# Performance work log

Hardware: AMD Instinct MI355X
Metric: run time of the kernel (lower is better)

The kernel has to match this reference:

```python
import jax, jax.numpy as jnp
import numpy as np

D_MODEL = 40
NUM_BUCKETS = 32
MAX_DISTANCE = 128
EPS = 1e-6


def rms_norm(x, w):
    # T5 LayerNorm: no mean subtraction, no bias
    var = jnp.mean(jnp.square(x), axis=-1, keepdims=True)
    return x * jax.lax.rsqrt(var + EPS) * w


def relative_position_bucket(rel, num_buckets=NUM_BUCKETS, max_distance=MAX_DISTANCE):
    # bidirectional (encoder) variant of T5's bucketing
    num_buckets = num_buckets // 2
    buckets = (rel > 0).astype(jnp.int32) * num_buckets
    rel = jnp.abs(rel)
    max_exact = num_buckets // 2
    is_small = rel < max_exact
    rel_f = jnp.maximum(rel, 1).astype(jnp.float32)
    large = max_exact + (
        jnp.log(rel_f / max_exact) / np.log(max_distance / max_exact) * (num_buckets - max_exact)
    ).astype(jnp.int32)
    large = jnp.minimum(large, num_buckets - 1)
    return buckets + jnp.where(is_small, rel, large)


def setup_inputs() -> dict:
    key = jax.random.key(0)
    ks = jax.random.split(key, 16)
    B, S, Din, D = 8, 2048, 128, D_MODEL
    w = lambda k, shape: (jax.random.normal(k, shape, dtype=jnp.float32) * 0.02)
    return {
        "embs": jax.random.normal(ks[0], (B, S, Din), dtype=jnp.float32),
        "Wa": w(ks[1], (Din, D)),
        "ba": jnp.zeros((D,), dtype=jnp.float32),
        "ln1": jnp.ones((D,), dtype=jnp.float32),
        "Wq": w(ks[2], (D, D)),
        "Wk": w(ks[3], (D, D)),
        "Wv": w(ks[4], (D, D)),
        "Wo": w(ks[5], (D, D)),
        "ln2": jnp.ones((D,), dtype=jnp.float32),
        "wi": w(ks[6], (D, D)),
        "wo": w(ks[7], (D, D)),
        "lnf": jnp.ones((D,), dtype=jnp.float32),
        "rel_bias": w(ks[8], (NUM_BUCKETS, 1)),  # [num_buckets, n_heads=1]
    }


def reference(embs, Wa, ba, ln1, Wq, Wk, Wv, Wo, ln2, wi, wo, lnf, rel_bias):
    # adapter
    x = jax.nn.relu(embs @ Wa + ba)  # [B,S,D]
    S = x.shape[1]

    # --- self-attention block (1 head, d_kv = d_model, no QK scaling) ---
    h = rms_norm(x, ln1)
    q = h @ Wq  # [B,S,D]
    k = h @ Wk
    v = h @ Wv

    pos = jnp.arange(S)
    rel = pos[None, :] - pos[:, None]           # memory - query, [S,S]
    buckets = relative_position_bucket(rel)      # [S,S]
    pos_bias = rel_bias[buckets][:, :, 0]        # [S,S], head dim squeezed (1 head)

    scores = jnp.einsum("bqd,bkd->bqk", q, k) + pos_bias[None]  # [B,S,S]
    attn = jax.nn.softmax(scores, axis=-1)
    o = jnp.einsum("bqk,bkd->bqd", attn, v) @ Wo
    x = x + o

    # --- feed-forward block ---
    h2 = rms_norm(x, ln2)
    f = jax.nn.relu(h2 @ wi) @ wo
    x = x + f

    return rms_norm(x, lnf)
```

## Files before the change

### kernel.cpp

```cpp
#include <hip/hip_runtime.h>
#include <hip/hip_bf16.h>
#include <math.h>

#define D 40
#define DIN 128
#define S 2048
#define B 8
#define NROWS (B*S)
#define DP 64
#define XSTR 48
#define PSTR 64
#define KSTR 72

typedef __bf16 bf16x8 __attribute__((ext_vector_type(8)));
typedef float f32x16 __attribute__((ext_vector_type(16)));

static __device__ __forceinline__ unsigned short f2bf(float f) {
    unsigned u = __builtin_bit_cast(unsigned, f);
    u += 0x7fff + ((u >> 16) & 1);
    return (unsigned short)(u >> 16);
}
static __device__ __forceinline__ float bf2f(unsigned short h) {
    return __builtin_bit_cast(float, (unsigned)h << 16);
}
static __device__ __forceinline__ bf16x8 ldfrag(const unsigned short* p) {
    return __builtin_bit_cast(bf16x8, *(const uint4*)p);
}
static __device__ __forceinline__ unsigned cvtpk(float lo, float hi) {
    unsigned r;
    asm("v_cvt_pk_bf16_f32 %0, %1, %2" : "=v"(r) : "v"(lo), "v"(hi));
    return r;
}
static __device__ __forceinline__ void plswap(unsigned &a, unsigned &b) {
    asm("v_permlane32_swap_b32 %0, %1" : "+v"(a), "+v"(b));
}

__global__ __launch_bounds__(256) void k0_prep(
    const float* __restrict__ Wa, const float* __restrict__ ba, const float* __restrict__ ln1,
    const float* __restrict__ Wq, const float* __restrict__ Wk, const float* __restrict__ Wv,
    const float* __restrict__ Wo, const float* __restrict__ ln2,
    const float* __restrict__ wi, const float* __restrict__ wo,
    const float* __restrict__ rel_bias,
    unsigned short* __restrict__ waT, unsigned short* __restrict__ wqT,
    unsigned short* __restrict__ wkT, unsigned short* __restrict__ wvT,
    unsigned short* __restrict__ woT, unsigned short* __restrict__ wiT,
    unsigned short* __restrict__ wo2T, float* __restrict__ btab)
{
    int i = blockIdx.x * 256 + threadIdx.x;
    if (i < 64*144) {
        int col = i / 144, k = i - col*144;
        float v = 0.f;
        if (col < D) {
            if (k < DIN) v = Wa[k*D + col];
            else if (k == DIN) v = ba[col];
        }
        waT[i] = f2bf(v);
    }
    if (i < 64*48) {
        int col = i / 48, d = i - col*48;
        bool ok = (col < D && d < D);
        float s1 = ok ? ln1[d] : 0.f;
        float s2 = ok ? ln2[d] : 0.f;
        wqT[i]  = f2bf(ok ? Wq[d*D + col] * s1 : 0.f);
        wkT[i]  = f2bf(ok ? Wk[d*D + col] * s1 : 0.f);
        wvT[i]  = f2bf(ok ? Wv[d*D + col] * s1 : 0.f);
        woT[i]  = f2bf(ok ? Wo[d*D + col]      : 0.f);
        wiT[i]  = f2bf(ok ? wi[d*D + col] * s2 : 0.f);
        wo2T[i] = f2bf(ok ? wo[d*D + col]      : 0.f);
    }
    if (i < 2*S - 1) {
        int rel = i - (S - 1);
        int bucket = (rel > 0) ? 16 : 0;
        int ar = rel < 0 ? -rel : rel;
        int add;
        if (ar < 8) {
            add = ar;
        } else {
            float tt = logf((float)ar * 0.125f) / logf(16.0f) * 8.0f;
            int lg = 8 + (int)tt;
            add = lg < 15 ? lg : 15;
        }
        btab[i] = rel_bias[bucket + add];
    }
}

static __device__ __forceinline__ void repack1(const f32x16& t0, uint4& u0, uint4& u1)
{
    unsigned a0=cvtpk(t0[0],t0[1]),  a1=cvtpk(t0[2],t0[3]),
             a2=cvtpk(t0[4],t0[5]),  a3=cvtpk(t0[6],t0[7]);
    plswap(a0,a2); plswap(a1,a3);
    unsigned b0=cvtpk(t0[8],t0[9]),  b1=cvtpk(t0[10],t0[11]),
             b2=cvtpk(t0[12],t0[13]),b3=cvtpk(t0[14],t0[15]);
    plswap(b0,b2); plswap(b1,b3);
    u0 = (uint4){a0,a1,a2,a3}; u1 = (uint4){b0,b1,b2,b3};
}

__global__ __launch_bounds__(128) void k1_adapter_qkv(
    const float* __restrict__ embs,
    const unsigned short* __restrict__ waT, const unsigned short* __restrict__ wqT,
    const unsigned short* __restrict__ wkT, const unsigned short* __restrict__ wvT,
    unsigned short* __restrict__ xb, unsigned short* __restrict__ qb,
    unsigned short* __restrict__ kbq, unsigned short* __restrict__ vT)
{
    __shared__ __attribute__((aligned(16))) unsigned short sE16[32][136];
    __shared__ unsigned short sX[32][56];
    __shared__ float sSS[2][32];

    const int tid = threadIdx.x;

    {
        int r = tid >> 2;
        int cc = (tid & 3) * 32;
        const float* src = embs + (size_t)(blockIdx.x*32 + r) * DIN + cc;
        #pragma unroll
        for (int i = 0; i < 4; ++i) {
            float4 f0 = *(const float4*)(src + i*8);
            float4 f1 = *(const float4*)(src + i*8 + 4);
            uint4 u = { cvtpk(f0.x, f0.y), cvtpk(f0.z, f0.w),
                        cvtpk(f1.x, f1.y), cvtpk(f1.z, f1.w) };
            *(uint4*)&sE16[r][cc + i*8] = u;
        }
    }
    __syncthreads();

    const int w   = tid >> 6;
    const int l   = tid & 63;
    const int lr  = l & 31, hi = l >> 5;
    const int row = blockIdx.x * 32 + lr;
    const int cb  = w * 32;

    bf16x8 eb[9];
    #pragma unroll
    for (int kk = 0; kk < 8; ++kk) eb[kk] = ldfrag(&sE16[lr][kk*16 + hi*8]);
    {
        uint4 u = { hi == 0 ? 0x3f80u : 0u, 0u, 0u, 0u };
        eb[8] = __builtin_bit_cast(bf16x8, u);
    }

    f32x16 x0 = {0,0,0,0,0,0,0,0,0,0,0,0,0,0,0,0};
    #pragma unroll
    for (int kk = 0; kk < 9; ++kk) {
        bf16x8 a0 = ldfrag(waT + (size_t)(cb + lr)*144 + kk*16 + hi*8);
        x0 = __builtin_amdgcn_mfma_f32_32x32x16_bf16(a0, eb[kk], x0, 0,0,0);
    }

    float ss = 0.f;
    #pragma unroll
    for (int r = 0; r < 16; ++r) {
        x0[r] = fmaxf(x0[r], 0.f);
        ss += x0[r]*x0[r];
    }
    ss += __shfl_xor(ss, 32);
    if (hi == 0) sSS[w][lr] = ss;
    __syncthreads();
    const float inv = rsqrtf((sSS[0][lr] + sSS[1][lr]) * (1.0f/D) + 1e-6f);

    {
        uint4 u0, u1; repack1(x0, u0, u1);
        unsigned short* p = xb + (size_t)row*XSTR;
        *(uint4*)(p + cb + hi*8) = u0;
        if (w == 0) *(uint4*)(p + 16 + hi*8) = u1;
    }

    f32x16 xh;
    #pragma unroll
    for (int r = 0; r < 16; ++r) xh[r] = x0[r] * inv;
    {
        uint4 u0, u1; repack1(xh, u0, u1);
        *(uint4*)(&sX[lr][cb + hi*8]) = u0;
        if (w == 0) *(uint4*)(&sX[lr][16 + hi*8]) = u1;
    }
    __syncthreads();
    bf16x8 hb[3];
    #pragma unroll
    for (int t = 0; t < 3; ++t) hb[t] = ldfrag(&sX[lr][t*16 + hi*8]);

    f32x16 qa={0,0,0,0,0,0,0,0,0,0,0,0,0,0,0,0};
    f32x16 ka={0,0,0,0,0,0,0,0,0,0,0,0,0,0,0,0};
    f32x16 va={0,0,0,0,0,0,0,0,0,0,0,0,0,0,0,0};
    #pragma unroll
    for (int t = 0; t < 3; ++t) {
        bf16x8 h = hb[t];
        qa = __builtin_amdgcn_mfma_f32_32x32x16_bf16(ldfrag(wqT + (size_t)(cb+lr)*48 + t*16 + hi*8), h, qa, 0,0,0);
        ka = __builtin_amdgcn_mfma_f32_32x32x16_bf16(ldfrag(wkT + (size_t)(cb+lr)*48 + t*16 + hi*8), h, ka, 0,0,0);
        va = __builtin_amdgcn_mfma_f32_32x32x16_bf16(ldfrag(wvT + (size_t)(cb+lr)*48 + t*16 + hi*8), h, va, 0,0,0);
    }

    {
        uint4 u0, u1; repack1(qa, u0, u1);
        unsigned short* p = qb + (size_t)row*DP;
        *(uint4*)(p + cb + hi*8) = u0;
        if (w == 0) *(uint4*)(p + 16 + hi*8) = u1;
    }
    {
        uint4 u0, u1; repack1(ka, u0, u1);
        unsigned short* p = kbq + (size_t)row*DP;
        *(uint4*)(p + cb + hi*8) = u0;
        if (w == 0) *(uint4*)(p + 16 + hi*8) = u1;
    }
    #pragma unroll
    for (int r = 0; r < 16; ++r) {
        int col = cb + (r&3) + 8*(r>>2) + 4*hi;
        vT[(size_t)col*NROWS + row] = f2bf(va[r]);
    }
}

__global__ __launch_bounds__(256, 2) void k3_attn_mfma(
    const unsigned short* __restrict__ qb, const unsigned short* __restrict__ kb,
    const unsigned short* __restrict__ vT, const float* __restrict__ btab,
    unsigned short* __restrict__ pob, float* __restrict__ pl, int klen, int nsplit)
{
    __shared__ float sbtw[2432];
    __shared__ __attribute__((aligned(16))) unsigned short sK[64][KSTR];
    __shared__ __attribute__((aligned(16))) unsigned short sV[64][KSTR];

    const int q0blk = blockIdx.x * 256;
    const int kt0   = blockIdx.z * klen;
    const int woff  = (S-1) + kt0 - q0blk - 255;

    int tid = threadIdx.x;
    for (int i = tid; i < klen + 256; i += 256) {
        int g = woff + i;
        sbtw[i] = btab[g < 0 ? 0 : (g > 4094 ? 4094 : g)];
    }

    const int w  = tid >> 6, l = tid & 63;
    const int lr = l & 31,  hi = l >> 5;
    const int b  = blockIdx.y;
    const int q0a = q0blk + w * 32;
    const int q0b = q0a + 128;

    const unsigned short* qrA = qb + ((size_t)(b*S) + q0a + lr) * DP + hi*8;
    bf16x8 qfA[3] = { ldfrag(qrA), ldfrag(qrA + 16), ldfrag(qrA + 32) };
    const unsigned short* qrB = qb + ((size_t)(b*S) + q0b + lr) * DP + hi*8;
    bf16x8 qfB[3] = { ldfrag(qrB), ldfrag(qrB + 16), ldfrag(qrB + 32) };

    f32x16 oA0 = {0,0,0,0,0,0,0,0,0,0,0,0,0,0,0,0};
    f32x16 oA1 = {0,0,0,0,0,0,0,0,0,0,0,0,0,0,0,0};
    f32x16 oB0 = {0,0,0,0,0,0,0,0,0,0,0,0,0,0,0,0};
    f32x16 oB1 = {0,0,0,0,0,0,0,0,0,0,0,0,0,0,0,0};
    float elA = 0.f, elB = 0.f;

    const int bbA = 255 - w*32 - lr + 4*hi;
    const int bbB = bbA - 128;

    const int srow = tid >> 3;
    const int scol = (tid & 7) * 8;

    auto stageRegs = [&](int kc, uint4& rk0, uint4& rk1, uint4& rv0, uint4& rv1) {
        const unsigned short* src = kb + (size_t)(b*S + kt0 + kc)*DP;
        rk0 = *(const uint4*)(src + (size_t)srow*DP + scol);
        rk1 = *(const uint4*)(src + (size_t)(32 + srow)*DP + scol);
        const unsigned short* vsrc = vT + (size_t)(b*S) + kt0 + kc;
        rv0 = *(const uint4*)(vsrc + (size_t)srow*NROWS + scol);
        rv1 = *(const uint4*)(vsrc + (size_t)(32 + srow)*NROWS + scol);
    };
    auto writeLds = [&](const uint4& rk0, const uint4& rk1, const uint4& rv0, const uint4& rv1) {
        *(uint4*)&sK[srow][scol]      = rk0;
        *(uint4*)&sK[32 + srow][scol] = rk1;
        *(uint4*)&sV[srow][scol]      = rv0;
        *(uint4*)&sV[32 + srow][scol] = rv1;
    };

    auto compute = [&](int ktl, int kloc, const bf16x8* qf,
                       f32x16& o0, f32x16& o1, float& el, int bb) {
        bf16x8 kf0 = ldfrag(&sK[kloc + lr][hi*8]);
        bf16x8 kf1 = ldfrag(&sK[kloc + lr][16 + hi*8]);
        bf16x8 kf2 = ldfrag(&sK[kloc + lr][32 + hi*8]);
        f32x16 c = {0,0,0,0,0,0,0,0,0,0,0,0,0,0,0,0};
        c = __builtin_amdgcn_mfma_f32_32x32x16_bf16(kf0, qf[0], c, 0,0,0);
        c = __builtin_amdgcn_mfma_f32_32x32x16_bf16(kf1, qf[1], c, 0,0,0);
        c = __builtin_amdgcn_mfma_f32_32x32x16_bf16(kf2, qf[2], c, 0,0,0);

        float e[16];
        #pragma unroll
        for (int r = 0; r < 16; ++r) {
            float s = c[r] + sbtw[bb + ktl + (r&3) + 8*(r>>2)];
            e[r] = __expf(s);
            el += e[r];
        }
        unsigned a0 = cvtpk(e[0],  e[1]);
        unsigned a1 = cvtpk(e[2],  e[3]);
        unsigned a2 = cvtpk(e[4],  e[5]);
        unsigned a3 = cvtpk(e[6],  e[7]);
        plswap(a0, a2);
        plswap(a1, a3);
        unsigned b0 = cvtpk(e[8],  e[9]);
        unsigned b1 = cvtpk(e[10], e[11]);
        unsigned b2 = cvtpk(e[12], e[13]);
        unsigned b3 = cvtpk(e[14], e[15]);
        plswap(b0, b2);
        plswap(b1, b3);
        uint4 u0 = {a0, a1, a2, a3};
        uint4 u1 = {b0, b1, b2, b3};
        bf16x8 pa0 = __builtin_bit_cast(bf16x8, u0);
        bf16x8 pa1 = __builtin_bit_cast(bf16x8, u1);

        bf16x8 vf0 = ldfrag(&sV[lr][kloc + hi*8]);
        bf16x8 vf1 = ldfrag(&sV[lr][kloc + 16 + hi*8]);
        bf16x8 vf2 = ldfrag(&sV[32 + lr][kloc + hi*8]);
        bf16x8 vf3 = ldfrag(&sV[32 + lr][kloc + 16 + hi*8]);

        o0 = __builtin_amdgcn_mfma_f32_32x32x16_bf16(pa0, vf0, o0, 0,0,0);
        o0 = __builtin_amdgcn_mfma_f32_32x32x16_bf16(pa1, vf1, o0, 0,0,0);
        o1 = __builtin_amdgcn_mfma_f32_32x32x16_bf16(pa0, vf2, o1, 0,0,0);
        o1 = __builtin_amdgcn_mfma_f32_32x32x16_bf16(pa1, vf3, o1, 0,0,0);
    };

    {
        uint4 rk0, rk1, rv0, rv1;
        stageRegs(0, rk0, rk1, rv0, rv1);
        writeLds(rk0, rk1, rv0, rv1);
    }
    __syncthreads();

    for (int kc = 0; kc < klen; kc += 64) {
        const bool more = (kc + 64 < klen);
        uint4 rk0, rk1, rv0, rv1;
        if (more) stageRegs(kc + 64, rk0, rk1, rv0, rv1);
        compute(kc,      0,  qfA, oA0, oA1, elA, bbA);
        compute(kc,      0,  qfB, oB0, oB1, elB, bbB);
        compute(kc + 32, 32, qfA, oA0, oA1, elA, bbA);
        compute(kc + 32, 32, qfB, oB0, oB1, elB, bbB);
        if (more) {
            __syncthreads();
            writeLds(rk0, rk1, rv0, rv1);
            __syncthreads();
        }
    }

    elA += __shfl_xor(elA, 32);
    elB += __shfl_xor(elB, 32);

    const size_t rbA = ((size_t)(b*S + q0a) * nsplit + blockIdx.z);
    const size_t rbB = ((size_t)(b*S + q0b) * nsplit + blockIdx.z);
    #pragma unroll
    for (int r = 0; r < 16; ++r) {
        int qr = (r&3) + 8*(r>>2) + 4*hi;
        unsigned short* prA = pob + (rbA + (size_t)qr * nsplit) * PSTR;
        prA[lr] = f2bf(oA0[r]);
        if (lr < 8) prA[32 + lr] = f2bf(oA1[r]);
        unsigned short* prB = pob + (rbB + (size_t)qr * nsplit) * PSTR;
        prB[lr] = f2bf(oB0[r]);
        if (lr < 8) prB[32 + lr] = f2bf(oB1[r]);
    }
    if (hi == 0) {
        pl[(size_t)blockIdx.z * NROWS + b*S + q0a + lr] = elA;
        pl[(size_t)blockIdx.z * NROWS + b*S + q0b + lr] = elB;
    }
}

__global__ __launch_bounds__(128) void k4_out_ff(
    const unsigned short* __restrict__ xb, const unsigned short* __restrict__ pob,
    const float* __restrict__ pl,
    const unsigned short* __restrict__ woT, const unsigned short* __restrict__ wiT,
    const unsigned short* __restrict__ wo2T, const float* __restrict__ lnf,
    float* __restrict__ out, int nsplit)
{
    __shared__ unsigned short sX[32][56];
    __shared__ float sSS[2][32];

    const int tid = threadIdx.x;
    const int w   = tid >> 6;
    const int l   = tid & 63;
    const int lr  = l & 31, hi = l >> 5;
    const int row = blockIdx.x * 32 + lr;
    const int cb  = w * 32;

    float lsum = 0.f;
    for (int s = 0; s < nsplit; ++s) lsum += pl[(size_t)s*NROWS + row];
    const float linv = 1.0f / lsum;

    float a[3][8];
    #pragma unroll
    for (int t = 0; t < 3; ++t)
        #pragma unroll
        for (int j = 0; j < 8; ++j) a[t][j] = 0.f;
    const unsigned short* prow = pob + (size_t)row * nsplit * PSTR;
    for (int s = 0; s < nsplit; ++s) {
        const unsigned short* pr = prow + (size_t)s * PSTR;
        #pragma unroll
        for (int t = 0; t < 3; ++t) {
            if (t == 2 && hi == 1) continue;
            uint4 u = *(const uint4*)(pr + t*16 + hi*8);
            a[t][0] += bf2f((unsigned short)(u.x)); a[t][1] += bf2f((unsigned short)(u.x >> 16));
            a[t][2] += bf2f((unsigned short)(u.y)); a[t][3] += bf2f((unsigned short)(u.y >> 16));
            a[t][4] += bf2f((unsigned short)(u.z)); a[t][5] += bf2f((unsigned short)(u.z >> 16));
            a[t][6] += bf2f((unsigned short)(u.w)); a[t][7] += bf2f((unsigned short)(u.w >> 16));
        }
    }
    bf16x8 ab[3];
    #pragma unroll
    for (int t = 0; t < 3; ++t) {
        uint4 u = { cvtpk(a[t][0]*linv, a[t][1]*linv), cvtpk(a[t][2]*linv, a[t][3]*linv),
                    cvtpk(a[t][4]*linv, a[t][5]*linv), cvtpk(a[t][6]*linv, a[t][7]*linv) };
        ab[t] = __builtin_bit_cast(bf16x8, u);
    }

    f32x16 c = {0,0,0,0,0,0,0,0,0,0,0,0,0,0,0,0};
    #pragma unroll
    for (int t = 0; t < 3; ++t)
        c = __builtin_amdgcn_mfma_f32_32x32x16_bf16(ldfrag(woT + (size_t)(cb+lr)*48 + t*16 + hi*8), ab[t], c, 0,0,0);

    const unsigned short* xr = xb + (size_t)row*XSTR;
    if (w == 0) {
        #pragma unroll
        for (int rr = 0; rr < 4; ++rr) {
            ushort4 v = *(const ushort4*)(xr + rr*8 + 4*hi);
            c[rr*4+0] += bf2f(v.x); c[rr*4+1] += bf2f(v.y);
            c[rr*4+2] += bf2f(v.z); c[rr*4+3] += bf2f(v.w);
        }
    } else {
        ushort4 v = *(const ushort4*)(xr + 32 + 4*hi);
        c[0] += bf2f(v.x); c[1] += bf2f(v.y); c[2] += bf2f(v.z); c[3] += bf2f(v.w);
    }

    float ss = 0.f;
    #pragma unroll
    for (int r = 0; r < 16; ++r) ss += c[r]*c[r];
    ss += __shfl_xor(ss, 32);
    if (hi == 0) sSS[w][lr] = ss;
    __syncthreads();
    const float inv2 = rsqrtf((sSS[0][lr] + sSS[1][lr]) * (1.0f/D) + 1e-6f);

    f32x16 t0;
    #pragma unroll
    for (int r = 0; r < 16; ++r) t0[r] = c[r]*inv2;
    {
        uint4 u0, u1; repack1(t0, u0, u1);
        *(uint4*)(&sX[lr][cb + hi*8]) = u0;
        if (w == 0) *(uint4*)(&sX[lr][16 + hi*8]) = u1;
    }
    __syncthreads();
    bf16x8 hb[3];
    #pragma unroll
    for (int t = 0; t < 3; ++t) hb[t] = ldfrag(&sX[lr][t*16 + hi*8]);
    __syncthreads();

    f32x16 d = {0,0,0,0,0,0,0,0,0,0,0,0,0,0,0,0};
    #pragma unroll
    for (int t = 0; t < 3; ++t)
        d = __builtin_amdgcn_mfma_f32_32x32x16_bf16(ldfrag(wiT + (size_t)(cb+lr)*48 + t*16 + hi*8), hb[t], d, 0,0,0);
    #pragma unroll
    for (int r = 0; r < 16; ++r) d[r] = fmaxf(d[r], 0.f);
    {
        uint4 u0, u1; repack1(d, u0, u1);
        *(uint4*)(&sX[lr][cb + hi*8]) = u0;
        if (w == 0) *(uint4*)(&sX[lr][16 + hi*8]) = u1;
    }
    __syncthreads();
    bf16x8 fb[3];
    #pragma unroll
    for (int t = 0; t < 3; ++t) fb[t] = ldfrag(&sX[lr][t*16 + hi*8]);

    f32x16 e = {0,0,0,0,0,0,0,0,0,0,0,0,0,0,0,0};
    #pragma unroll
    for (int t = 0; t < 3; ++t)
        e = __builtin_amdgcn_mfma_f32_32x32x16_bf16(ldfrag(wo2T + (size_t)(cb+lr)*48 + t*16 + hi*8), fb[t], e, 0,0,0);
    #pragma unroll
    for (int r = 0; r < 16; ++r) e[r] += c[r];

    float ss2 = 0.f;
    #pragma unroll
    for (int r = 0; r < 16; ++r) ss2 += e[r]*e[r];
    ss2 += __shfl_xor(ss2, 32);
    if (hi == 0) sSS[w][lr] = ss2;
    __syncthreads();
    const float inv3 = rsqrtf((sSS[0][lr] + sSS[1][lr]) * (1.0f/D) + 1e-6f);

    float* orow = out + (size_t)row * D;
    if (w == 0) {
        #pragma unroll
        for (int rr = 0; rr < 4; ++rr) {
            float4 lf = *(const float4*)(lnf + rr*8 + 4*hi);
            float4 v = { e[rr*4+0]*inv3*lf.x, e[rr*4+1]*inv3*lf.y,
                         e[rr*4+2]*inv3*lf.z, e[rr*4+3]*inv3*lf.w };
            *(float4*)(orow + rr*8 + 4*hi) = v;
        }
    } else {
        float4 lf = *(const float4*)(lnf + 32 + 4*hi);
        float4 v = { e[0]*inv3*lf.x, e[1]*inv3*lf.y, e[2]*inv3*lf.z, e[3]*inv3*lf.w };
        *(float4*)(orow + 32 + 4*hi) = v;
    }
}

extern "C" void kernel_launch(void* const* d_in, const int* in_sizes, int n_in,
                              void* d_out, int out_size, void* d_ws, size_t ws_size,
                              hipStream_t stream) {
    const float* embs = (const float*)d_in[0];
    const float* Wa   = (const float*)d_in[1];
    const float* ba   = (const float*)d_in[2];
    const float* ln1  = (const float*)d_in[3];
    const float* Wq   = (const float*)d_in[4];
    const float* Wk   = (const float*)d_in[5];
    const float* Wv   = (const float*)d_in[6];
    const float* Wo   = (const float*)d_in[7];
    const float* ln2  = (const float*)d_in[8];
    const float* wi   = (const float*)d_in[9];
    const float* wo   = (const float*)d_in[10];
    const float* lnf  = (const float*)d_in[11];
    const float* rb   = (const float*)d_in[12];

    char* wsb = (char*)d_ws;
    unsigned short* xb   = (unsigned short*)(wsb);
    unsigned short* qb   = (unsigned short*)(wsb + 1572864);
    unsigned short* kbq  = (unsigned short*)(wsb + 3670016);
    unsigned short* vT   = (unsigned short*)(wsb + 5767168);
    unsigned short* waT  = (unsigned short*)(wsb + 7864320);
    unsigned short* wqT  = (unsigned short*)(wsb + 7882752);
    unsigned short* wkT  = (unsigned short*)(wsb + 7888896);
    unsigned short* wvT  = (unsigned short*)(wsb + 7895040);
    unsigned short* woT  = (unsigned short*)(wsb + 7901184);
    unsigned short* wiT  = (unsigned short*)(wsb + 7907328);
    unsigned short* wo2T = (unsigned short*)(wsb + 7913472);
    const size_t base = 7919616;

    int nsplit = 8;
    while (nsplit > 1 &&
           base + (size_t)nsplit*(2097152 + 65536) + 16384 > ws_size)
        nsplit >>= 1;
    unsigned short* pob = (unsigned short*)(wsb + base);
    float* pl   = (float*)(wsb + base + (size_t)nsplit*2097152);
    float* btab = (float*)(wsb + base + (size_t)nsplit*(2097152 + 65536));
    int klen = S / nsplit;

    k0_prep<<<36, 256, 0, stream>>>(Wa, ba, ln1, Wq, Wk, Wv, Wo, ln2, wi, wo, rb,
                                    waT, wqT, wkT, wvT, woT, wiT, wo2T, btab);
    k1_adapter_qkv<<<NROWS/32, 128, 0, stream>>>(embs, waT, wqT, wkT, wvT, xb, qb, kbq, vT);
    k3_attn_mfma<<<dim3(S/256, B, nsplit), 256, 0, stream>>>(qb, kbq, vT, btab, pob, pl, klen, nsplit);
    k4_out_ff<<<NROWS/32, 128, 0, stream>>>(xb, pob, pl, woT, wiT, wo2T, lnf, (float*)d_out, nsplit);
}
```

Before: 44.86 us.

## Double-buffer K/V LDS tiles and pack softmax row sums into partial outputs

The attention kernel now keeps two LDS buffers for K and V, so the next tile is written into the spare buffer and each iteration needs one barrier instead of two. The per-split softmax denominators move out of the separate pl array and into the unused padding slots (elements 40-41) of each partial-output row. The combine kernel then reads the sum and the partial output from the same cache line, and one workspace buffer goes away. The cost is doubled K/V LDS footprint, which may reduce occupancy, and scattered 16-bit stores for the sums.

```diff
diff --git a/kernel.cpp b/kernel.cpp
--- a/kernel.cpp
+++ b/kernel.cpp
@@ -208,11 +208,11 @@
 __global__ __launch_bounds__(256, 2) void k3_attn_mfma(
     const unsigned short* __restrict__ qb, const unsigned short* __restrict__ kb,
     const unsigned short* __restrict__ vT, const float* __restrict__ btab,
-    unsigned short* __restrict__ pob, float* __restrict__ pl, int klen, int nsplit)
+    unsigned short* __restrict__ pob, int klen, int nsplit)
 {
     __shared__ float sbtw[2432];
-    __shared__ __attribute__((aligned(16))) unsigned short sK[64][KSTR];
-    __shared__ __attribute__((aligned(16))) unsigned short sV[64][KSTR];
+    __shared__ __attribute__((aligned(16))) unsigned short sK[2][64][KSTR];
+    __shared__ __attribute__((aligned(16))) unsigned short sV[2][64][KSTR];
 
     const int q0blk = blockIdx.x * 256;
     const int kt0   = blockIdx.z * klen;
@@ -255,18 +255,18 @@
         rv0 = *(const uint4*)(vsrc + (size_t)srow*NROWS + scol);
         rv1 = *(const uint4*)(vsrc + (size_t)(32 + srow)*NROWS + scol);
     };
-    auto writeLds = [&](const uint4& rk0, const uint4& rk1, const uint4& rv0, const uint4& rv1) {
-        *(uint4*)&sK[srow][scol]      = rk0;
-        *(uint4*)&sK[32 + srow][scol] = rk1;
-        *(uint4*)&sV[srow][scol]      = rv0;
-        *(uint4*)&sV[32 + srow][scol] = rv1;
+    auto writeLds = [&](int bf, const uint4& rk0, const uint4& rk1, const uint4& rv0, const uint4& rv1) {
+        *(uint4*)&sK[bf][srow][scol]      = rk0;
+        *(uint4*)&sK[bf][32 + srow][scol] = rk1;
+        *(uint4*)&sV[bf][srow][scol]      = rv0;
+        *(uint4*)&sV[bf][32 + srow][scol] = rv1;
     };
 
-    auto compute = [&](int ktl, int kloc, const bf16x8* qf,
+    auto compute = [&](int ktl, int kloc, int bf, const bf16x8* qf,
                        f32x16& o0, f32x16& o1, float& el, int bb) {
-        bf16x8 kf0 = ldfrag(&sK[kloc + lr][hi*8]);
-        bf16x8 kf1 = ldfrag(&sK[kloc + lr][16 + hi*8]);
-        bf16x8 kf2 = ldfrag(&sK[kloc + lr][32 + hi*8]);
+        bf16x8 kf0 = ldfrag(&sK[bf][kloc + lr][hi*8]);
+        bf16x8 kf1 = ldfrag(&sK[bf][kloc + lr][16 + hi*8]);
+        bf16x8 kf2 = ldfrag(&sK[bf][kloc + lr][32 + hi*8]);
         f32x16 c = {0,0,0,0,0,0,0,0,0,0,0,0,0,0,0,0};
         c = __builtin_amdgcn_mfma_f32_32x32x16_bf16(kf0, qf[0], c, 0,0,0);
         c = __builtin_amdgcn_mfma_f32_32x32x16_bf16(kf1, qf[1], c, 0,0,0);
@@ -296,10 +296,10 @@
         bf16x8 pa0 = __builtin_bit_cast(bf16x8, u0);
         bf16x8 pa1 = __builtin_bit_cast(bf16x8, u1);
 
-        bf16x8 vf0 = ldfrag(&sV[lr][kloc + hi*8]);
-        bf16x8 vf1 = ldfrag(&sV[lr][kloc + 16 + hi*8]);
-        bf16x8 vf2 = ldfrag(&sV[32 + lr][kloc + hi*8]);
-        bf16x8 vf3 = ldfrag(&sV[32 + lr][kloc + 16 + hi*8]);
+        bf16x8 vf0 = ldfrag(&sV[bf][lr][kloc + hi*8]);
+        bf16x8 vf1 = ldfrag(&sV[bf][lr][kloc + 16 + hi*8]);
+        bf16x8 vf2 = ldfrag(&sV[bf][32 + lr][kloc + hi*8]);
+        bf16x8 vf3 = ldfrag(&sV[bf][32 + lr][kloc + 16 + hi*8]);
 
         o0 = __builtin_amdgcn_mfma_f32_32x32x16_bf16(pa0, vf0, o0, 0,0,0);
         o0 = __builtin_amdgcn_mfma_f32_32x32x16_bf16(pa1, vf1, o0, 0,0,0);
@@ -310,22 +310,23 @@
     {
         uint4 rk0, rk1, rv0, rv1;
         stageRegs(0, rk0, rk1, rv0, rv1);
-        writeLds(rk0, rk1, rv0, rv1);
-    }
-    __syncthreads();
-
+        writeLds(0, rk0, rk1, rv0, rv1);
+    }
+    __syncthreads();
+
+    int buf = 0;
     for (int kc = 0; kc < klen; kc += 64) {
         const bool more = (kc + 64 < klen);
         uint4 rk0, rk1, rv0, rv1;
         if (more) stageRegs(kc + 64, rk0, rk1, rv0, rv1);
-        compute(kc,      0,  qfA, oA0, oA1, elA, bbA);
-        compute(kc,      0,  qfB, oB0, oB1, elB, bbB);
-        compute(kc + 32, 32, qfA, oA0, oA1, elA, bbA);
-        compute(kc + 32, 32, qfB, oB0, oB1, elB, bbB);
+        compute(kc,      0,  buf, qfA, oA0, oA1, elA, bbA);
+        compute(kc,      0,  buf, qfB, oB0, oB1, elB, bbB);
+        compute(kc + 32, 32, buf, qfA, oA0, oA1, elA, bbA);
+        compute(kc + 32, 32, buf, qfB, oB0, oB1, elB, bbB);
         if (more) {
+            writeLds(buf ^ 1, rk0, rk1, rv0, rv1);
             __syncthreads();
-            writeLds(rk0, rk1, rv0, rv1);
-            __syncthreads();
+            buf ^= 1;
         }
     }
 
@@ -345,14 +346,17 @@
         if (lr < 8) prB[32 + lr] = f2bf(oB1[r]);
     }
     if (hi == 0) {
-        pl[(size_t)blockIdx.z * NROWS + b*S + q0a + lr] = elA;
-        pl[(size_t)blockIdx.z * NROWS + b*S + q0b + lr] = elB;
+        unsigned ea = __builtin_bit_cast(unsigned, elA);
+        unsigned short* prA = pob + (rbA + (size_t)lr * nsplit) * PSTR;
+        prA[40] = (unsigned short)ea; prA[41] = (unsigned short)(ea >> 16);
+        unsigned eb2 = __builtin_bit_cast(unsigned, elB);
+        unsigned short* prB = pob + (rbB + (size_t)lr * nsplit) * PSTR;
+        prB[40] = (unsigned short)eb2; prB[41] = (unsigned short)(eb2 >> 16);
     }
 }
 
 __global__ __launch_bounds__(128) void k4_out_ff(
     const unsigned short* __restrict__ xb, const unsigned short* __restrict__ pob,
-    const float* __restrict__ pl,
     const unsigned short* __restrict__ woT, const unsigned short* __restrict__ wiT,
     const unsigned short* __restrict__ wo2T, const float* __restrict__ lnf,
     float* __restrict__ out, int nsplit)
@@ -368,9 +372,6 @@
     const int cb  = w * 32;
 
     float lsum = 0.f;
-    for (int s = 0; s < nsplit; ++s) lsum += pl[(size_t)s*NROWS + row];
-    const float linv = 1.0f / lsum;
-
     float a[3][8];
     #pragma unroll
     for (int t = 0; t < 3; ++t)
@@ -379,6 +380,8 @@
     const unsigned short* prow = pob + (size_t)row * nsplit * PSTR;
     for (int s = 0; s < nsplit; ++s) {
         const unsigned short* pr = prow + (size_t)s * PSTR;
+        unsigned eu = (unsigned)pr[40] | ((unsigned)pr[41] << 16);
+        lsum += __builtin_bit_cast(float, eu);
         #pragma unroll
         for (int t = 0; t < 3; ++t) {
             if (t == 2 && hi == 1) continue;
@@ -389,6 +392,7 @@
             a[t][6] += bf2f((unsigned short)(u.w)); a[t][7] += bf2f((unsigned short)(u.w >> 16));
         }
     }
+    const float linv = 1.0f / lsum;
     bf16x8 ab[3];
     #pragma unroll
     for (int t = 0; t < 3; ++t) {
@@ -517,16 +521,15 @@
 
     int nsplit = 8;
     while (nsplit > 1 &&
-           base + (size_t)nsplit*(2097152 + 65536) + 16384 > ws_size)
+           base + (size_t)nsplit*2097152 + 16384 > ws_size)
         nsplit >>= 1;
     unsigned short* pob = (unsigned short*)(wsb + base);
-    float* pl   = (float*)(wsb + base + (size_t)nsplit*2097152);
-    float* btab = (float*)(wsb + base + (size_t)nsplit*(2097152 + 65536));
+    float* btab = (float*)(wsb + base + (size_t)nsplit*2097152);
     int klen = S / nsplit;
 
     k0_prep<<<36, 256, 0, stream>>>(Wa, ba, ln1, Wq, Wk, Wv, Wo, ln2, wi, wo, rb,
                                     waT, wqT, wkT, wvT, woT, wiT, wo2T, btab);
     k1_adapter_qkv<<<NROWS/32, 128, 0, stream>>>(embs, waT, wqT, wkT, wvT, xb, qb, kbq, vT);
-    k3_attn_mfma<<<dim3(S/256, B, nsplit), 256, 0, stream>>>(qb, kbq, vT, btab, pob, pl, klen, nsplit);
-    k4_out_ff<<<NROWS/32, 128, 0, stream>>>(xb, pob, pl, woT, wiT, wo2T, lnf, (float*)d_out, nsplit);
-}
+    k3_attn_mfma<<<dim3(S/256, B, nsplit), 256, 0, stream>>>(qb, kbq, vT, btab, pob, klen, nsplit);
+    k4_out_ff<<<NROWS/32, 128, 0, stream>>>(xb, pob, woT, wiT, wo2T, lnf, (float*)d_out, nsplit);
+}
```

Result: faster. 43.09 us (-3.9%).
